# Performance work log

Measured on AMD Instinct MI355X. Metric: run time of the kernel, lower is better.

Reference implementation:

```python
import jax, jax.numpy as jnp
import numpy as np

B, W, D = 8, 1024, 1024
HEADS, KDIM, VDIM = 16, 64, 64


def setup_inputs() -> dict:
    key = jax.random.key(0)
    k1, k2, k3, k4 = jax.random.split(key, 4)
    # he_normal-ish scaling for weights
    s = (2.0 / D) ** 0.5
    return {
        "inputs": jax.random.normal(k1, (B, W, D), dtype=jnp.float32),
        "Wq": jax.random.normal(k2, (D, HEADS * KDIM), dtype=jnp.float32) * s,
        "Wk": jax.random.normal(k3, (D, HEADS * KDIM), dtype=jnp.float32) * s,
        "Wv": jax.random.normal(k4, (D, HEADS * VDIM), dtype=jnp.float32) * s,
    }


def reference(inputs, Wq, Wk, Wv):
    # Self-attention: memory = inputs
    bsz, win, _ = inputs.shape
    # DenseHeads: linear projection, reshaped to (B, W, heads, head_units)
    q = (inputs @ Wq).reshape(bsz, win, HEADS, KDIM)
    k = (inputs @ Wk).reshape(bsz, win, HEADS, KDIM)
    v = (inputs @ Wv).reshape(bsz, win, HEADS, VDIM)
    scale = KDIM ** (-0.5)
    # scores[b,q,h,m] = sum_k Q[b,q,h,k] * K[b,m,h,k]
    scores = jnp.einsum("bqhk,bmhk->bqhm", q, k) * scale
    attn = jax.nn.softmax(scores, axis=-1)
    # out[b,q,h,v] = sum_m attn[b,q,h,m] * V[b,m,h,v]
    out = jnp.einsum("bqhm,bmhv->bqhv", attn, v)
    return out
```

## Files before the change

### kernel.cpp

```cpp
#include <hip/hip_runtime.h>
#include <stdint.h>


using bf16x8 = __attribute__((ext_vector_type(8))) __bf16;
using f32x4  = __attribute__((ext_vector_type(4))) float;

union frag_u { uint4 u4; bf16x8 f; };

__device__ inline unsigned short f2bf(float x){
  unsigned int u = __float_as_uint(x);
  u += 0x7fffu + ((u >> 16) & 1u);
  return (unsigned short)(u >> 16);
}

__device__ inline void gl_lds16(const void* g, void* l){
  __builtin_amdgcn_global_load_lds(
      (const __attribute__((address_space(1))) void*)g,
      (__attribute__((address_space(3))) void*)l, 16, 0, 0);
}

__global__ void cast_x(const float* __restrict__ X, unsigned short* __restrict__ Xb){
  int i = (blockIdx.x * 256 + threadIdx.x) * 4;
  float4 v = *(const float4*)(X + i);
  ushort4 o;
  o.x = f2bf(v.x); o.y = f2bf(v.y); o.z = f2bf(v.z); o.w = f2bf(v.w);
  *(ushort4*)(Xb + i) = o;
}

__global__ void cast_wt(const float* __restrict__ Wq, const float* __restrict__ Wk,
                        const float* __restrict__ Wv, unsigned short* __restrict__ Wt){
  __shared__ float tile[64][65];
  int id = blockIdx.x;
  int proj = id >> 8;
  int rem  = id & 255;
  int kt = rem & 15, nt = rem >> 4;
  const float* Wsrc = (proj == 0) ? Wq : ((proj == 1) ? Wk : Wv);
  int k0 = kt * 64, n0 = nt * 64;
  int tx = threadIdx.x & 63, ty = threadIdx.x >> 6;
  for (int i = 0; i < 16; i++){
    int k = i * 4 + ty;
    tile[k][tx] = Wsrc[(k0 + k) * 1024 + n0 + tx];
  }
  __syncthreads();
  for (int i = 0; i < 16; i++){
    int n = i * 4 + ty;
    Wt[(proj * 1024 + n0 + n) * 1024 + k0 + tx] = f2bf(tile[tx][n]);
  }
}

__global__ void gemm_qkv(const unsigned short* __restrict__ Xb,
                         const unsigned short* __restrict__ Wt,
                         unsigned short* __restrict__ QKV){
  __shared__ __align__(16) unsigned short Abuf[128 * 64];
  __shared__ __align__(16) unsigned short Bbuf[128 * 64];
  int bid = blockIdx.x;
  int bx = bid % 24, by = bid / 24;
  int w = threadIdx.x >> 6, lane = threadIdx.x & 63;
  int g = lane >> 4, li = lane & 15;
  int lrow = lane >> 3, lcol = lane & 7;
  int wm = (w >> 1) * 64, wn = (w & 1) * 64;
  f32x4 acc[4][4] = {};

  for (int k0 = 0; k0 < 1024; k0 += 64){
    __syncthreads();
    for (int i = 0; i < 4; i++){
      int idx = w * 4 + i;
      int row = idx * 8 + lrow;
      gl_lds16(Xb + (by * 128 + row) * 1024 + k0 + lcol * 8, Abuf + idx * 512);
      gl_lds16(Wt + (bx * 128 + row) * 1024 + k0 + lcol * 8, Bbuf + idx * 512);
    }
    __syncthreads();
    for (int c = 0; c < 2; c++){
      frag_u a[4], b[4];
      for (int i = 0; i < 4; i++)
        a[i].u4 = *(const uint4*)(Abuf + (wm + i * 16 + li) * 64 + c * 32 + g * 8);
      for (int j = 0; j < 4; j++)
        b[j].u4 = *(const uint4*)(Bbuf + (wn + j * 16 + li) * 64 + c * 32 + g * 8);
      for (int i = 0; i < 4; i++)
        for (int j = 0; j < 4; j++)
          acc[i][j] = __builtin_amdgcn_mfma_f32_16x16x32_bf16(a[i].f, b[j].f, acc[i][j], 0, 0, 0);
    }
  }
  float sc = (bx < 8) ? 0.1803368801111f : 1.0f;
  for (int i = 0; i < 4; i++){
    int row = by * 128 + wm + i * 16 + g * 4;
    for (int j = 0; j < 4; j++){
      int col = bx * 128 + wn + j * 16 + li;
      for (int r = 0; r < 4; r++)
        QKV[(row + r) * 3072 + col] = f2bf(acc[i][j][r] * sc);
    }
  }
}

__global__ void vtrans(const unsigned short* __restrict__ QKV, unsigned short* __restrict__ Vt){
  __shared__ unsigned short tile[64][66];
  int id = blockIdx.x;
  int bh = id >> 4, mt = id & 15;
  int b = bh >> 4, h = bh & 15;
  int m0 = mt * 64;
  int tx = threadIdx.x & 63, ty = threadIdx.x >> 6;
  for (int i = 0; i < 16; i++){
    int r = i * 4 + ty;
    tile[r][tx] = QKV[(b * 1024 + m0 + r) * 3072 + 2048 + h * 64 + tx];
  }
  __syncthreads();
  for (int i = 0; i < 16; i++){
    int d = i * 4 + ty;
    Vt[bh * 65536 + d * 1024 + m0 + tx] = tile[tx][d];
  }
}

__global__ void attn(const unsigned short* __restrict__ QKV,
                     const unsigned short* __restrict__ Vt,
                     float* __restrict__ Out){
  __shared__ __align__(16) unsigned short Kbuf[64 * 64];
  __shared__ __align__(16) unsigned short Vbuf[64 * 64];
  __shared__ __align__(16) unsigned short Pbuf[4][16 * 88];
  int id = blockIdx.x;
  int bh = id >> 4, qb = id & 15;
  int b = bh >> 4, h = bh & 15;
  int w = threadIdx.x >> 6, lane = threadIdx.x & 63;
  int g = lane >> 4, li = lane & 15;
  int lrow = lane >> 3, lcol = lane & 7;
  int scol = ((lcol ^ lrow) & 7) * 8;

  frag_u qf[2];
  {
    int tok = b * 1024 + qb * 64 + w * 16 + li;
    const unsigned short* qp = QKV + (size_t)tok * 3072 + h * 64 + g * 8;
    qf[0].u4 = *(const uint4*)(qp);
    qf[1].u4 = *(const uint4*)(qp + 32);
  }

  f32x4 o[4] = {};
  float psum = 0.f;

  const unsigned short* Kg = QKV + (size_t)(b * 1024) * 3072 + 1024 + h * 64;
  const unsigned short* Vg = Vt + (size_t)bh * 65536;
  unsigned short* pb = &Pbuf[w][0];

  for (int mt = 0; mt < 16; mt++){
    int m0 = mt * 64;
    __syncthreads();
    for (int i = 0; i < 2; i++){
      int idx = w * 2 + i;
      int row = idx * 8 + lrow;
      gl_lds16(Kg + (size_t)(m0 + row) * 3072 + scol, Kbuf + idx * 512);
      gl_lds16(Vg + row * 1024 + m0 + scol, Vbuf + idx * 512);
    }
    __syncthreads();

    f32x4 s[4] = {};
    for (int t = 0; t < 4; t++){
      for (int c = 0; c < 2; c++){
        frag_u kf;
        kf.u4 = *(const uint4*)(Kbuf + (t * 16 + li) * 64 + ((((c << 2) + g) ^ (li & 7)) << 3));
        s[t] = __builtin_amdgcn_mfma_f32_16x16x32_bf16(kf.f, qf[c].f, s[t], 0, 0, 0);
      }
    }

    for (int t = 0; t < 4; t++){
      float p0 = __builtin_exp2f(s[t][0]);
      float p1 = __builtin_exp2f(s[t][1]);
      float p2 = __builtin_exp2f(s[t][2]);
      float p3 = __builtin_exp2f(s[t][3]);
      psum += (p0 + p1) + (p2 + p3);
      ushort4 pk;
      pk.x = f2bf(p0); pk.y = f2bf(p1); pk.z = f2bf(p2); pk.w = f2bf(p3);
      *(ushort4*)(pb + li * 88 + t * 16 + g * 4) = pk;
    }
    asm volatile("s_waitcnt lgkmcnt(0)" ::: "memory");

    frag_u pf[2];
    pf[0].u4 = *(const uint4*)(pb + li * 88 + g * 8);
    pf[1].u4 = *(const uint4*)(pb + li * 88 + 32 + g * 8);
    for (int t = 0; t < 4; t++){
      for (int c = 0; c < 2; c++){
        frag_u vf;
        vf.u4 = *(const uint4*)(Vbuf + (t * 16 + li) * 64 + ((((c << 2) + g) ^ (li & 7)) << 3));
        o[t] = __builtin_amdgcn_mfma_f32_16x16x32_bf16(vf.f, pf[c].f, o[t], 0, 0, 0);
      }
    }
  }

  psum += __shfl_xor(psum, 16);
  psum += __shfl_xor(psum, 32);
  float inv = 1.f / psum;

  int tok = b * 1024 + qb * 64 + w * 16 + li;
  float* op = Out + (size_t)tok * 1024 + h * 64 + g * 4;
  for (int t = 0; t < 4; t++){
    float4 v4;
    v4.x = o[t][0] * inv; v4.y = o[t][1] * inv;
    v4.z = o[t][2] * inv; v4.w = o[t][3] * inv;
    *(float4*)(op + t * 16) = v4;
  }
}

extern "C" void kernel_launch(void* const* d_in, const int* in_sizes, int n_in,
                              void* d_out, int out_size, void* d_ws, size_t ws_size,
                              hipStream_t stream) {
  const float* X  = (const float*)d_in[0];
  const float* Wq = (const float*)d_in[1];
  const float* Wk = (const float*)d_in[2];
  const float* Wv = (const float*)d_in[3];
  float* Out = (float*)d_out;
  char* ws = (char*)d_ws;
  unsigned short* Xb  = (unsigned short*)(ws);
  unsigned short* Wt  = (unsigned short*)(ws + (size_t)16 * 1024 * 1024);
  unsigned short* QKV = (unsigned short*)(ws + (size_t)22 * 1024 * 1024);
  unsigned short* Vt  = (unsigned short*)(ws + (size_t)70 * 1024 * 1024);

  cast_x  <<<8192, 256, 0, stream>>>(X, Xb);
  cast_wt <<<768,  256, 0, stream>>>(Wq, Wk, Wv, Wt);
  gemm_qkv<<<1536, 256, 0, stream>>>(Xb, Wt, QKV);
  vtrans  <<<2048, 256, 0, stream>>>(QKV, Vt);
  attn    <<<2048, 256, 0, stream>>>(QKV, Vt, Out);
}
```

Measured before the change: 229.3 us.

## Fuse V transpose into QKV GEMM epilogue and give attention waves two query tiles

The GEMM epilogue now writes the V projection directly in transposed per-head layout, which removes the separate vtrans kernel and its extra read/write pass over V. Q and K are stored in a narrower 2048-column buffer. Each attention wave now handles 32 query rows instead of 16, reusing each loaded K/V fragment for two MFMAs and halving the grid. P values are also packed into bf16 pairs with a hardware convert builtin where one is available. The cost is more registers per wave and fewer blocks, which may lower occupancy.

```diff
diff --git a/kernel.cpp b/kernel.cpp
--- a/kernel.cpp
+++ b/kernel.cpp
@@ -11,6 +11,15 @@
   unsigned int u = __float_as_uint(x);
   u += 0x7fffu + ((u >> 16) & 1u);
   return (unsigned short)(u >> 16);
+}
+
+__device__ inline unsigned int pack2bf(float a, float b){
+#if __has_builtin(__builtin_amdgcn_cvt_pk_bf16_f32)
+  auto r = __builtin_amdgcn_cvt_pk_bf16_f32(a, b);
+  unsigned int u; __builtin_memcpy(&u, &r, 4); return u;
+#else
+  return (unsigned int)f2bf(a) | ((unsigned int)f2bf(b) << 16);
+#endif
 }
 
 __device__ inline void gl_lds16(const void* g, void* l){
@@ -50,7 +59,8 @@
 
 __global__ void gemm_qkv(const unsigned short* __restrict__ Xb,
                          const unsigned short* __restrict__ Wt,
-                         unsigned short* __restrict__ QKV){
+                         unsigned short* __restrict__ QK,
+                         unsigned short* __restrict__ Vt){
   __shared__ __align__(16) unsigned short Abuf[128 * 64];
   __shared__ __align__(16) unsigned short Bbuf[128 * 64];
   int bid = blockIdx.x;
@@ -81,61 +91,58 @@
           acc[i][j] = __builtin_amdgcn_mfma_f32_16x16x32_bf16(a[i].f, b[j].f, acc[i][j], 0, 0, 0);
     }
   }
-  float sc = (bx < 8) ? 0.1803368801111f : 1.0f;
-  for (int i = 0; i < 4; i++){
-    int row = by * 128 + wm + i * 16 + g * 4;
-    for (int j = 0; j < 4; j++){
-      int col = bx * 128 + wn + j * 16 + li;
-      for (int r = 0; r < 4; r++)
-        QKV[(row + r) * 3072 + col] = f2bf(acc[i][j][r] * sc);
-    }
-  }
-}
-
-__global__ void vtrans(const unsigned short* __restrict__ QKV, unsigned short* __restrict__ Vt){
-  __shared__ unsigned short tile[64][66];
-  int id = blockIdx.x;
-  int bh = id >> 4, mt = id & 15;
-  int b = bh >> 4, h = bh & 15;
-  int m0 = mt * 64;
-  int tx = threadIdx.x & 63, ty = threadIdx.x >> 6;
-  for (int i = 0; i < 16; i++){
-    int r = i * 4 + ty;
-    tile[r][tx] = QKV[(b * 1024 + m0 + r) * 3072 + 2048 + h * 64 + tx];
-  }
-  __syncthreads();
-  for (int i = 0; i < 16; i++){
-    int d = i * 4 + ty;
-    Vt[bh * 65536 + d * 1024 + m0 + tx] = tile[tx][d];
-  }
-}
-
-__global__ void attn(const unsigned short* __restrict__ QKV,
-                     const unsigned short* __restrict__ Vt,
-                     float* __restrict__ Out){
+  if (bx >= 16){
+    for (int i = 0; i < 4; i++){
+      int row = by * 128 + wm + i * 16 + g * 4;
+      int bb = row >> 10, m = row & 1023;
+      for (int j = 0; j < 4; j++){
+        int vc = bx * 128 + wn + j * 16 + li - 2048;
+        int hh = vc >> 6, dd = vc & 63;
+        ushort4 pk;
+        pk.x = f2bf(acc[i][j][0]); pk.y = f2bf(acc[i][j][1]);
+        pk.z = f2bf(acc[i][j][2]); pk.w = f2bf(acc[i][j][3]);
+        *(ushort4*)(Vt + ((size_t)(bb * 16 + hh) * 64 + dd) * 1024 + m) = pk;
+      }
+    }
+  } else {
+    float sc = (bx < 8) ? 0.1803368801111f : 1.0f;
+    for (int i = 0; i < 4; i++){
+      int row = by * 128 + wm + i * 16 + g * 4;
+      for (int j = 0; j < 4; j++){
+        int col = bx * 128 + wn + j * 16 + li;
+        for (int r = 0; r < 4; r++)
+          QK[(size_t)(row + r) * 2048 + col] = f2bf(acc[i][j][r] * sc);
+      }
+    }
+  }
+}
+
+__global__ __launch_bounds__(256) void attn(const unsigned short* __restrict__ QK,
+                                            const unsigned short* __restrict__ Vt,
+                                            float* __restrict__ Out){
   __shared__ __align__(16) unsigned short Kbuf[64 * 64];
   __shared__ __align__(16) unsigned short Vbuf[64 * 64];
-  __shared__ __align__(16) unsigned short Pbuf[4][16 * 88];
+  __shared__ __align__(16) unsigned short Pbuf[4][32 * 88];
   int id = blockIdx.x;
-  int bh = id >> 4, qb = id & 15;
+  int bh = id >> 3, qb = id & 7;
   int b = bh >> 4, h = bh & 15;
   int w = threadIdx.x >> 6, lane = threadIdx.x & 63;
   int g = lane >> 4, li = lane & 15;
   int lrow = lane >> 3, lcol = lane & 7;
   int scol = ((lcol ^ lrow) & 7) * 8;
 
-  frag_u qf[2];
-  {
-    int tok = b * 1024 + qb * 64 + w * 16 + li;
-    const unsigned short* qp = QKV + (size_t)tok * 3072 + h * 64 + g * 8;
-    qf[0].u4 = *(const uint4*)(qp);
-    qf[1].u4 = *(const uint4*)(qp + 32);
-  }
-
-  f32x4 o[4] = {};
-  float psum = 0.f;
-
-  const unsigned short* Kg = QKV + (size_t)(b * 1024) * 3072 + 1024 + h * 64;
+  frag_u qf[2][2];
+  for (int u = 0; u < 2; u++){
+    int tok = b * 1024 + qb * 128 + w * 32 + u * 16 + li;
+    const unsigned short* qp = QK + (size_t)tok * 2048 + h * 64 + g * 8;
+    qf[u][0].u4 = *(const uint4*)(qp);
+    qf[u][1].u4 = *(const uint4*)(qp + 32);
+  }
+
+  f32x4 o[2][4] = {};
+  float psum[2] = {0.f, 0.f};
+
+  const unsigned short* Kg = QK + (size_t)b * 1024 * 2048 + 1024 + h * 64;
   const unsigned short* Vg = Vt + (size_t)bh * 65536;
   unsigned short* pb = &Pbuf[w][0];
 
@@ -145,55 +152,66 @@
     for (int i = 0; i < 2; i++){
       int idx = w * 2 + i;
       int row = idx * 8 + lrow;
-      gl_lds16(Kg + (size_t)(m0 + row) * 3072 + scol, Kbuf + idx * 512);
+      gl_lds16(Kg + (size_t)(m0 + row) * 2048 + scol, Kbuf + idx * 512);
       gl_lds16(Vg + row * 1024 + m0 + scol, Vbuf + idx * 512);
     }
     __syncthreads();
 
-    f32x4 s[4] = {};
+    f32x4 s[2][4] = {};
     for (int t = 0; t < 4; t++){
       for (int c = 0; c < 2; c++){
         frag_u kf;
         kf.u4 = *(const uint4*)(Kbuf + (t * 16 + li) * 64 + ((((c << 2) + g) ^ (li & 7)) << 3));
-        s[t] = __builtin_amdgcn_mfma_f32_16x16x32_bf16(kf.f, qf[c].f, s[t], 0, 0, 0);
-      }
-    }
-
-    for (int t = 0; t < 4; t++){
-      float p0 = __builtin_exp2f(s[t][0]);
-      float p1 = __builtin_exp2f(s[t][1]);
-      float p2 = __builtin_exp2f(s[t][2]);
-      float p3 = __builtin_exp2f(s[t][3]);
-      psum += (p0 + p1) + (p2 + p3);
-      ushort4 pk;
-      pk.x = f2bf(p0); pk.y = f2bf(p1); pk.z = f2bf(p2); pk.w = f2bf(p3);
-      *(ushort4*)(pb + li * 88 + t * 16 + g * 4) = pk;
+        s[0][t] = __builtin_amdgcn_mfma_f32_16x16x32_bf16(kf.f, qf[0][c].f, s[0][t], 0, 0, 0);
+        s[1][t] = __builtin_amdgcn_mfma_f32_16x16x32_bf16(kf.f, qf[1][c].f, s[1][t], 0, 0, 0);
+      }
+    }
+
+    for (int u = 0; u < 2; u++){
+      for (int t = 0; t < 4; t++){
+        float p0 = __builtin_exp2f(s[u][t][0]);
+        float p1 = __builtin_exp2f(s[u][t][1]);
+        float p2 = __builtin_exp2f(s[u][t][2]);
+        float p3 = __builtin_exp2f(s[u][t][3]);
+        psum[u] += (p0 + p1) + (p2 + p3);
+        uint2 pk;
+        pk.x = pack2bf(p0, p1);
+        pk.y = pack2bf(p2, p3);
+        *(uint2*)(pb + (u * 16 + li) * 88 + t * 16 + g * 4) = pk;
+      }
     }
     asm volatile("s_waitcnt lgkmcnt(0)" ::: "memory");
 
-    frag_u pf[2];
-    pf[0].u4 = *(const uint4*)(pb + li * 88 + g * 8);
-    pf[1].u4 = *(const uint4*)(pb + li * 88 + 32 + g * 8);
+    frag_u pf[2][2];
+    for (int u = 0; u < 2; u++){
+      pf[u][0].u4 = *(const uint4*)(pb + (u * 16 + li) * 88 + g * 8);
+      pf[u][1].u4 = *(const uint4*)(pb + (u * 16 + li) * 88 + 32 + g * 8);
+    }
     for (int t = 0; t < 4; t++){
       for (int c = 0; c < 2; c++){
         frag_u vf;
         vf.u4 = *(const uint4*)(Vbuf + (t * 16 + li) * 64 + ((((c << 2) + g) ^ (li & 7)) << 3));
-        o[t] = __builtin_amdgcn_mfma_f32_16x16x32_bf16(vf.f, pf[c].f, o[t], 0, 0, 0);
-      }
-    }
-  }
-
-  psum += __shfl_xor(psum, 16);
-  psum += __shfl_xor(psum, 32);
-  float inv = 1.f / psum;
-
-  int tok = b * 1024 + qb * 64 + w * 16 + li;
-  float* op = Out + (size_t)tok * 1024 + h * 64 + g * 4;
-  for (int t = 0; t < 4; t++){
-    float4 v4;
-    v4.x = o[t][0] * inv; v4.y = o[t][1] * inv;
-    v4.z = o[t][2] * inv; v4.w = o[t][3] * inv;
-    *(float4*)(op + t * 16) = v4;
+        o[0][t] = __builtin_amdgcn_mfma_f32_16x16x32_bf16(vf.f, pf[0][c].f, o[0][t], 0, 0, 0);
+        o[1][t] = __builtin_amdgcn_mfma_f32_16x16x32_bf16(vf.f, pf[1][c].f, o[1][t], 0, 0, 0);
+      }
+    }
+  }
+
+  for (int u = 0; u < 2; u++){
+    psum[u] += __shfl_xor(psum[u], 16);
+    psum[u] += __shfl_xor(psum[u], 32);
+  }
+
+  for (int u = 0; u < 2; u++){
+    float inv = 1.f / psum[u];
+    int tok = b * 1024 + qb * 128 + w * 32 + u * 16 + li;
+    float* op = Out + (size_t)tok * 1024 + h * 64 + g * 4;
+    for (int t = 0; t < 4; t++){
+      float4 v4;
+      v4.x = o[u][t][0] * inv; v4.y = o[u][t][1] * inv;
+      v4.z = o[u][t][2] * inv; v4.w = o[u][t][3] * inv;
+      *(float4*)(op + t * 16) = v4;
+    }
   }
 }
 
@@ -206,14 +224,13 @@
   const float* Wv = (const float*)d_in[3];
   float* Out = (float*)d_out;
   char* ws = (char*)d_ws;
-  unsigned short* Xb  = (unsigned short*)(ws);
-  unsigned short* Wt  = (unsigned short*)(ws + (size_t)16 * 1024 * 1024);
-  unsigned short* QKV = (unsigned short*)(ws + (size_t)22 * 1024 * 1024);
-  unsigned short* Vt  = (unsigned short*)(ws + (size_t)70 * 1024 * 1024);
+  unsigned short* Xb = (unsigned short*)(ws);
+  unsigned short* Wt = (unsigned short*)(ws + (size_t)16 * 1024 * 1024);
+  unsigned short* QK = (unsigned short*)(ws + (size_t)22 * 1024 * 1024);
+  unsigned short* Vt = (unsigned short*)(ws + (size_t)54 * 1024 * 1024);
 
   cast_x  <<<8192, 256, 0, stream>>>(X, Xb);
   cast_wt <<<768,  256, 0, stream>>>(Wq, Wk, Wv, Wt);
-  gemm_qkv<<<1536, 256, 0, stream>>>(Xb, Wt, QKV);
-  vtrans  <<<2048, 256, 0, stream>>>(QKV, Vt);
-  attn    <<<2048, 256, 0, stream>>>(QKV, Vt, Out);
-}
+  gemm_qkv<<<1536, 256, 0, stream>>>(Xb, Wt, QK, Vt);
+  attn    <<<1024, 256, 0, stream>>>(QK, Vt, Out);
+}
```

Result: no change. 225.6 us (-1.6%).
